# Kernel optimization log

Measured on AMD Instinct MI355X. Metric: run time of the kernel, lower is better.

The kernel has to match this reference:

```python
import jax, jax.numpy as jnp
import numpy as np

EPS = 1e-6

def _rms_norm(t, g):
    # t: [B, S, C] (applied before the view to heads, matching the torch code)
    y = t.astype(jnp.float32)
    y = jax.lax.rsqrt(jnp.mean(y * y, axis=-1, keepdims=True) + EPS)
    return (t * y * g).astype(t.dtype)

def _apply_rope(t, cos, sin):
    # t: [B, S, N, D]; cos/sin: [1, S, 1, D//2]; interleaved pair rotation
    b, s, n, d = t.shape
    tr = t.reshape(b, s, n, d // 2, 2)
    tre, tim = tr[..., 0], tr[..., 1]
    out = jnp.stack([tre * cos - tim * sin, tre * sin + tim * cos], axis=-1)
    return out.reshape(b, s, n, d)

def setup_inputs() -> dict:
    key = jax.random.key(0)
    ks = jax.random.split(key, 8)
    B, S, DIM, N, D = 2, 1024, 3072, 24, 128
    x = jax.random.normal(ks[0], (B, S, DIM), dtype=jnp.float32)
    seq_lens = jax.random.randint(ks[1], (B,), S // 2, S + 1, dtype=jnp.int32)
    grid_sizes = jnp.tile(jnp.array([[16, 8, 8]], dtype=jnp.int32), (B, 1))
    # rope angle table [1024, D//2]: pos * inv_freq
    inv_freq = 1.0 / (10000.0 ** (jnp.arange(D // 2, dtype=jnp.float32) * 2.0 / D))
    freqs = jnp.arange(1024, dtype=jnp.float32)[:, None] * inv_freq[None, :]
    sc = 1.0 / np.sqrt(DIM)
    Wq = jax.random.normal(ks[2], (DIM, DIM), dtype=jnp.float32) * sc
    Wk = jax.random.normal(ks[3], (DIM, DIM), dtype=jnp.float32) * sc
    Wv = jax.random.normal(ks[4], (DIM, DIM), dtype=jnp.float32) * sc
    Wo = jax.random.normal(ks[5], (DIM, DIM), dtype=jnp.float32) * sc
    bq = jnp.zeros((DIM,), jnp.float32); bk = jnp.zeros((DIM,), jnp.float32)
    bv = jnp.zeros((DIM,), jnp.float32); bo = jnp.zeros((DIM,), jnp.float32)
    gq = jnp.ones((DIM,), jnp.float32); gk = jnp.ones((DIM,), jnp.float32)
    return {"x": x, "seq_lens": seq_lens, "grid_sizes": grid_sizes, "freqs": freqs,
            "Wq": Wq, "bq": bq, "Wk": Wk, "bk": bk, "Wv": Wv, "bv": bv,
            "Wo": Wo, "bo": bo, "gq": gq, "gk": gk}

def reference(x, seq_lens, grid_sizes, freqs, Wq, bq, Wk, bk, Wv, bv, Wo, bo, gq, gk):
    b, s, dim = x.shape
    d = 2 * freqs.shape[1]          # head_dim
    n = dim // d                    # num_heads
    q = _rms_norm(x @ Wq.T + bq, gq).reshape(b, s, n, d)
    k = _rms_norm(x @ Wk.T + bk, gk).reshape(b, s, n, d)
    v = (x @ Wv.T + bv).reshape(b, s, n, d)
    ang = freqs[:s]                 # [S, D//2]
    cos = jnp.cos(ang)[None, :, None, :]
    sin = jnp.sin(ang)[None, :, None, :]
    q = _apply_rope(q, cos, sin)
    k = _apply_rope(k, cos, sin)
    # full attention (window_size = (-1,-1)), varlen key masking via seq_lens
    scale = d ** -0.5
    scores = jnp.einsum('bind,bjnd->bnij', q, k) * scale   # [B,N,S,S]
    key_valid = jnp.arange(s)[None, :] < seq_lens[:, None]  # [B,S]
    scores = jnp.where(key_valid[:, None, None, :], scores, jnp.finfo(scores.dtype).min)
    p = jax.nn.softmax(scores, axis=-1)
    out = jnp.einsum('bnij,bjnd->bind', p, v).reshape(b, s, dim)
    return out @ Wo.T + bo
```

## Files before the change

### kernel.cpp

```cpp
#include <hip/hip_runtime.h>
#include <cmath>

#define BB   2
#define SS   1024
#define DIMM 3072
#define NHH  24
#define HDD  128
#define MM   (BB * SS)

typedef _Float16 f16;
typedef __attribute__((ext_vector_type(8))) _Float16 half8;
typedef __attribute__((ext_vector_type(4))) float floatx4;
typedef unsigned int u32;
typedef const __attribute__((address_space(1))) u32* gp1;
typedef __attribute__((address_space(3))) u32* lp3;

__device__ __forceinline__ void gload_lds16(const void* g, void* l) {
    __builtin_amdgcn_global_load_lds((gp1)g, (lp3)l, 16, 0, 0);
}

__global__ __launch_bounds__(256) void cvt_f16_kernel(
    const float* __restrict__ in, f16* __restrict__ outp, int n8)
{
    int i = blockIdx.x * 256 + threadIdx.x;
    if (i >= n8) return;
    const float4* p = (const float4*)(in + (size_t)i * 8);
    float4 a = p[0], b = p[1];
    half8 h = {(f16)a.x, (f16)a.y, (f16)a.z, (f16)a.w,
               (f16)b.x, (f16)b.y, (f16)b.z, (f16)b.w};
    *(half8*)(outp + (size_t)i * 8) = h;
}

template<bool QKV>
__global__ __launch_bounds__(256) void gemm_f16(
    const f16* __restrict__ A,
    const float* __restrict__ W0, const float* __restrict__ W1, const float* __restrict__ W2,
    const float* __restrict__ b0, const float* __restrict__ b1, const float* __restrict__ b2,
    f16* __restrict__ D0, f16* __restrict__ D1, f16* __restrict__ D2,
    float* __restrict__ F)
{
    constexpr int K = DIMM;
    constexpr int NSTEP = K / 32;
    __shared__ f16 As[128 * 32];
    __shared__ f16 Bs[128 * 32];

    const int tid  = threadIdx.x;
    const int lane = tid & 63;
    const int wave = tid >> 6;
    const int wm = wave >> 1, wn = wave & 1;
    const int lr = lane & 15;
    const int lq = lane >> 4;

    const int id  = blockIdx.x;
    const int cpx = (int)gridDim.x >> 3;
    const int swz = (id & 7) * cpx + (id >> 3);
    const int bm = (swz & 15) << 7;
    const int bn = (swz >> 4) << 7;

    const float* W; const float* bias; f16* D = nullptr;
    int nloc = bn;
    if constexpr (QKV) {
        int sel = bn / DIMM;
        nloc = bn - sel * DIMM;
        W    = sel == 0 ? W0 : (sel == 1 ? W1 : W2);
        bias = sel == 0 ? b0 : (sel == 1 ? b1 : b2);
        D    = sel == 0 ? D0 : (sel == 1 ? D1 : D2);
    } else { W = W0; bias = b0; }

    const int r0 = tid >> 2;
    const int c8 = (tid & 3) << 3;
    const float* bp0 = W + (size_t)(nloc + r0) * K + c8;
    const float* bp1 = W + (size_t)(nloc + r0 + 64) * K + c8;

    const int arow_l = lane >> 2;
    const int acol_l = (lane & 3) << 3;
    const f16* agbase = A + (size_t)bm * K;

    float4 sb00, sb01, sb10, sb11;
    auto LOADB = [&](int k0) {
        sb00 = *(const float4*)(bp0 + k0); sb01 = *(const float4*)(bp0 + k0 + 4);
        sb10 = *(const float4*)(bp1 + k0); sb11 = *(const float4*)(bp1 + k0 + 4);
    };
    auto STOREB = [&]() {
        half8 h0 = {(f16)sb00.x, (f16)sb00.y, (f16)sb00.z, (f16)sb00.w,
                    (f16)sb01.x, (f16)sb01.y, (f16)sb01.z, (f16)sb01.w};
        half8 h1 = {(f16)sb10.x, (f16)sb10.y, (f16)sb10.z, (f16)sb10.w,
                    (f16)sb11.x, (f16)sb11.y, (f16)sb11.z, (f16)sb11.w};
        *(half8*)&Bs[r0 * 32 + c8]        = h0;
        *(half8*)&Bs[(r0 + 64) * 32 + c8] = h1;
    };

    floatx4 acc[4][4];
#pragma unroll
    for (int i = 0; i < 4; ++i)
#pragma unroll
        for (int j = 0; j < 4; ++j) acc[i][j] = (floatx4){0.f, 0.f, 0.f, 0.f};

    LOADB(0);
    for (int ks = 0; ks < NSTEP; ++ks) {
        const int k0 = ks * 32;
        __syncthreads();
#pragma unroll
        for (int i = 0; i < 2; ++i) {
            int rbase = wave * 32 + i * 16;
            gload_lds16(agbase + (size_t)(rbase + arow_l) * K + k0 + acol_l,
                        &As[rbase * 32]);
        }
        STOREB();
        __syncthreads();
        if (ks + 1 < NSTEP) LOADB(k0 + 32);

        half8 af[4], bf[4];
#pragma unroll
        for (int i = 0; i < 4; ++i) {
            af[i] = *(const half8*)&As[(wm * 64 + i * 16 + lr) * 32 + lq * 8];
            bf[i] = *(const half8*)&Bs[(wn * 64 + i * 16 + lr) * 32 + lq * 8];
        }
#pragma unroll
        for (int mi = 0; mi < 4; ++mi)
#pragma unroll
            for (int ni = 0; ni < 4; ++ni)
                acc[mi][ni] = __builtin_amdgcn_mfma_f32_16x16x32_f16(af[mi], bf[ni], acc[mi][ni], 0, 0, 0);
    }

    const int crow0 = bm + wm * 64 + (lq << 2);
    const int ccol0 = nloc + wn * 64;
#pragma unroll
    for (int ni = 0; ni < 4; ++ni) {
        const int col = ccol0 + ni * 16 + lr;
        const float bv = bias[col];
#pragma unroll
        for (int mi = 0; mi < 4; ++mi) {
            const int row = crow0 + mi * 16;
#pragma unroll
            for (int r2 = 0; r2 < 4; ++r2) {
                if constexpr (QKV)
                    D[(size_t)(row + r2) * DIMM + col] = (f16)(acc[mi][ni][r2] + bv);
                else
                    F[(size_t)(row + r2) * DIMM + col] = acc[mi][ni][r2] + bv;
            }
        }
    }
}

__global__ __launch_bounds__(192) void rmsnorm_rope_f16(
    f16* __restrict__ q, f16* __restrict__ k,
    const float* __restrict__ gq, const float* __restrict__ gk,
    const float* __restrict__ freqs)
{
    f16* t = (blockIdx.y == 0) ? q : k;
    const float* g = (blockIdx.y == 0) ? gq : gk;
    const int row = blockIdx.x;
    const int s = row & (SS - 1);
    const int tid = threadIdx.x;
    f16* base = t + (size_t)row * DIMM + tid * 16;

    half8 v0 = *(const half8*)base;
    half8 v1 = *(const half8*)(base + 8);
    float v[16];
#pragma unroll
    for (int j = 0; j < 8; ++j) { v[j] = (float)v0[j]; v[8 + j] = (float)v1[j]; }

    float ssq = 0.f;
#pragma unroll
    for (int j = 0; j < 16; ++j) ssq += v[j] * v[j];
#pragma unroll
    for (int off = 32; off > 0; off >>= 1) ssq += __shfl_down(ssq, off, 64);
    __shared__ float red[3];
    if ((tid & 63) == 0) red[tid >> 6] = ssq;
    __syncthreads();
    float tot = red[0] + red[1] + red[2];
    float sc = rsqrtf(tot * (1.0f / (float)DIMM) + 1e-6f);

    const float* gp = g + tid * 16;
    float y[16];
#pragma unroll
    for (int j = 0; j < 16; ++j) y[j] = v[j] * sc * gp[j];

#pragma unroll
    for (int p = 0; p < 8; ++p) {
        int idx = tid * 16 + 2 * p;
        int f = (idx & 127) >> 1;
        float ang = freqs[s * 64 + f];
        float cc = cosf(ang), sn = sinf(ang);
        float e = y[2 * p], o = y[2 * p + 1];
        y[2 * p]     = e * cc - o * sn;
        y[2 * p + 1] = e * sn + o * cc;
    }
    half8 o0, o1;
#pragma unroll
    for (int j = 0; j < 8; ++j) { o0[j] = (f16)y[j]; o1[j] = (f16)y[8 + j]; }
    *(half8*)base       = o0;
    *(half8*)(base + 8) = o1;
}

__global__ __launch_bounds__(256) void flash_attn_f16(
    const f16* __restrict__ Q, const f16* __restrict__ K,
    const f16* __restrict__ V, const int* __restrict__ seq_lens,
    f16* __restrict__ O)
{
    __shared__ f16 QPs[64 * 128];
    __shared__ f16 Ks[64 * 128];
    __shared__ f16 Vt[128 * 64];

    const int tid  = threadIdx.x;
    const int lane = tid & 63;
    const int wave = tid >> 6;
    const int ln = lane & 15;
    const int lq = lane >> 4;
    const int i0 = blockIdx.x * 64;
    const int h  = blockIdx.y;
    const int b  = blockIdx.z;
    const int slen = seq_lens[b];
    const float scale = 0.08838834764831845f;
    const size_t gstride = NHH * HDD;

    const f16* Qg = Q + ((size_t)(b * SS + i0) * NHH + h) * HDD;
#pragma unroll
    for (int rep = 0; rep < 4; ++rep) {
        int u = tid + rep * 256;
        int r = u >> 4, d0 = (u & 15) << 3;
        half8 qv = *(const half8*)(Qg + (size_t)r * gstride + d0);
        *(half8*)(QPs + r * 128 + (d0 ^ ((r & 7) << 3))) = qv;
    }
    __syncthreads();

    half8 qfrag[4];
    {
        int rq = wave * 16 + ln;
#pragma unroll
        for (int ks = 0; ks < 4; ++ks)
            qfrag[ks] = *(const half8*)(QPs + rq * 128 + ((ks * 32 + lq * 8) ^ ((rq & 7) << 3)));
    }

    floatx4 accO[8];
#pragma unroll
    for (int dt = 0; dt < 8; ++dt) accO[dt] = (floatx4){0.f, 0.f, 0.f, 0.f};
    float mrow[4] = {-3.0e38f, -3.0e38f, -3.0e38f, -3.0e38f};
    float lrow[4] = {0.f, 0.f, 0.f, 0.f};

    const int nT = (slen + 63) >> 6;
    for (int t = 0; t < nT; ++t) {
        const int j0g = t * 64;
        __syncthreads();

        const f16* Kg = K + ((size_t)(b * SS + j0g) * NHH + h) * HDD;
#pragma unroll
        for (int rep = 0; rep < 4; ++rep) {
            int u = tid + rep * 256;
            int r = u >> 4, d0 = (u & 15) << 3;
            half8 kv = *(const half8*)(Kg + (size_t)r * gstride + d0);
            *(half8*)(Ks + r * 128 + (d0 ^ ((r & 7) << 3))) = kv;
        }
        const f16* Vg = V + ((size_t)(b * SS + j0g) * NHH + h) * HDD;
#pragma unroll
        for (int rep = 0; rep < 2; ++rep) {
            int u = tid + rep * 256;
            int jp = u & 31, j0 = jp * 2;
            int d0 = (u >> 5) << 3;
            half8 va = *(const half8*)(Vg + (size_t)j0 * gstride + d0);
            half8 vb = *(const half8*)(Vg + (size_t)(j0 + 1) * gstride + d0);
#pragma unroll
            for (int i = 0; i < 8; ++i) {
                int d = d0 + i;
                union { f16 h[2]; u32 w; } pk;
                pk.h[0] = va[i]; pk.h[1] = vb[i];
                *(u32*)(Vt + d * 64 + (j0 ^ ((d & 7) << 3))) = pk.w;
            }
        }
        __syncthreads();

        floatx4 acc_s[4];
#pragma unroll
        for (int nt = 0; nt < 4; ++nt) {
            acc_s[nt] = (floatx4){0.f, 0.f, 0.f, 0.f};
            int rk = nt * 16 + ln;
#pragma unroll
            for (int ks = 0; ks < 4; ++ks) {
                half8 kf = *(const half8*)(Ks + rk * 128 + ((ks * 32 + lq * 8) ^ ((rk & 7) << 3)));
                acc_s[nt] = __builtin_amdgcn_mfma_f32_16x16x32_f16(qfrag[ks], kf, acc_s[nt], 0, 0, 0);
            }
        }

        float s[4][4];
#pragma unroll
        for (int nt = 0; nt < 4; ++nt) {
            int j = j0g + nt * 16 + ln;
            bool valid = (j < slen);
#pragma unroll
            for (int r = 0; r < 4; ++r)
                s[nt][r] = valid ? acc_s[nt][r] * scale : -3.0e38f;
        }
        float fct[4];
#pragma unroll
        for (int r = 0; r < 4; ++r) {
            float m4 = fmaxf(fmaxf(s[0][r], s[1][r]), fmaxf(s[2][r], s[3][r]));
            m4 = fmaxf(m4, __shfl_xor(m4, 1, 64));
            m4 = fmaxf(m4, __shfl_xor(m4, 2, 64));
            m4 = fmaxf(m4, __shfl_xor(m4, 4, 64));
            m4 = fmaxf(m4, __shfl_xor(m4, 8, 64));
            float mn = fmaxf(mrow[r], m4);
            fct[r] = __expf(mrow[r] - mn);
            mrow[r] = mn;
            float ls = 0.f;
#pragma unroll
            for (int nt = 0; nt < 4; ++nt) {
                float p = __expf(s[nt][r] - mn);
                s[nt][r] = p;
                ls += p;
            }
            ls += __shfl_xor(ls, 1, 64);
            ls += __shfl_xor(ls, 2, 64);
            ls += __shfl_xor(ls, 4, 64);
            ls += __shfl_xor(ls, 8, 64);
            lrow[r] = lrow[r] * fct[r] + ls;
        }

#pragma unroll
        for (int nt = 0; nt < 4; ++nt) {
#pragma unroll
            for (int r = 0; r < 4; ++r) {
                int rw = lq * 4 + r;
                int j = nt * 16 + ln;
                QPs[(wave * 16 + rw) * 128 + (j ^ ((rw & 7) << 3))] = (f16)s[nt][r];
            }
        }

#pragma unroll
        for (int dt = 0; dt < 8; ++dt)
#pragma unroll
            for (int r = 0; r < 4; ++r) accO[dt][r] *= fct[r];

        half8 pfrag[2];
#pragma unroll
        for (int js = 0; js < 2; ++js)
            pfrag[js] = *(const half8*)(QPs + (wave * 16 + ln) * 128 + ((js * 32 + lq * 8) ^ ((ln & 7) << 3)));
#pragma unroll
        for (int dt = 0; dt < 8; ++dt) {
            int d = dt * 16 + ln;
#pragma unroll
            for (int js = 0; js < 2; ++js) {
                half8 vf = *(const half8*)(Vt + d * 64 + ((js * 32 + lq * 8) ^ ((d & 7) << 3)));
                accO[dt] = __builtin_amdgcn_mfma_f32_16x16x32_f16(pfrag[js], vf, accO[dt], 0, 0, 0);
            }
        }
    }

    float linv[4];
#pragma unroll
    for (int r = 0; r < 4; ++r) linv[r] = 1.0f / lrow[r];
    f16* Og = O + ((size_t)(b * SS + i0) * NHH + h) * HDD;
#pragma unroll
    for (int dt = 0; dt < 8; ++dt) {
#pragma unroll
        for (int r = 0; r < 4; ++r) {
            int qr = wave * 16 + lq * 4 + r;
            int d = dt * 16 + ln;
            Og[(size_t)qr * gstride + d] = (f16)(accO[dt][r] * linv[r]);
        }
    }
}

extern "C" void kernel_launch(void* const* d_in, const int* in_sizes, int n_in,
                              void* d_out, int out_size, void* d_ws, size_t ws_size,
                              hipStream_t stream)
{
    const float* x     = (const float*)d_in[0];
    const int*   seq   = (const int*)d_in[1];
    const float* freqs = (const float*)d_in[3];
    const float* Wq    = (const float*)d_in[4];
    const float* bq    = (const float*)d_in[5];
    const float* Wk    = (const float*)d_in[6];
    const float* bk    = (const float*)d_in[7];
    const float* Wv    = (const float*)d_in[8];
    const float* bv    = (const float*)d_in[9];
    const float* Wo    = (const float*)d_in[10];
    const float* bo    = (const float*)d_in[11];
    const float* gq    = (const float*)d_in[12];
    const float* gk    = (const float*)d_in[13];

    float* out = (float*)d_out;
    const size_t MD = (size_t)MM * DIMM;

    f16* X16 = (f16*)d_ws;
    f16* q16 = X16 + MD;
    f16* k16 = X16 + 2 * MD;
    f16* v16 = (f16*)d_out;

    cvt_f16_kernel<<<(int)(MD / (256 * 8)), 256, 0, stream>>>(x, X16, (int)(MD / 8));
    gemm_f16<true><<<(MM / 128) * (3 * DIMM / 128), 256, 0, stream>>>(
        X16, Wq, Wk, Wv, bq, bk, bv, q16, k16, v16, nullptr);
    rmsnorm_rope_f16<<<dim3(MM, 2), 192, 0, stream>>>(q16, k16, gq, gk, freqs);
    flash_attn_f16<<<dim3(SS / 64, NHH, BB), 256, 0, stream>>>(q16, k16, v16, seq, X16);
    gemm_f16<false><<<(MM / 128) * (DIMM / 128), 256, 0, stream>>>(
        X16, Wo, nullptr, nullptr, bo, nullptr, nullptr, nullptr, nullptr, nullptr, out);
}
```

Before: 386.7 us.

## Pre-convert weights to f16 and use direct-to-LDS GEMM with swizzled tiles

After: 368.8 us. -4.6%, faster.

```diff
diff --git a/kernel.cpp b/kernel.cpp
--- a/kernel.cpp
+++ b/kernel.cpp
@@ -32,7 +32,103 @@
 }
 
 template<bool QKV>
-__global__ __launch_bounds__(256) void gemm_f16(
+__global__ __launch_bounds__(256) void gemm_f16p(
+    const f16* __restrict__ A,
+    const f16* __restrict__ W0, const f16* __restrict__ W1, const f16* __restrict__ W2,
+    const float* __restrict__ b0, const float* __restrict__ b1, const float* __restrict__ b2,
+    f16* __restrict__ D0, f16* __restrict__ D1, f16* __restrict__ D2,
+    float* __restrict__ F)
+{
+    constexpr int K = DIMM;
+    constexpr int NSTEP = K / 64;
+    __shared__ __align__(16) f16 As[128 * 64];
+    __shared__ __align__(16) f16 Bs[128 * 64];
+
+    const int tid  = threadIdx.x;
+    const int lane = tid & 63;
+    const int wave = tid >> 6;
+    const int wm = wave >> 1, wn = wave & 1;
+    const int lr = lane & 15;
+    const int lq = lane >> 4;
+
+    const int id  = blockIdx.x;
+    const int cpx = (int)gridDim.x >> 3;
+    const int swz = (id & 7) * cpx + (id >> 3);
+    const int bm = (swz & 15) << 7;
+    const int bn = (swz >> 4) << 7;
+
+    const f16* Wh; const float* bias; f16* D = nullptr;
+    int nloc = bn;
+    if constexpr (QKV) {
+        int sel = bn / DIMM;
+        nloc = bn - sel * DIMM;
+        Wh   = sel == 0 ? W0 : (sel == 1 ? W1 : W2);
+        bias = sel == 0 ? b0 : (sel == 1 ? b1 : b2);
+        D    = sel == 0 ? D0 : (sel == 1 ? D1 : D2);
+    } else { Wh = W0; bias = b0; }
+
+    const int srow = lane >> 3;
+    const int scol = ((lane & 7) ^ srow) << 3;
+    const f16* ag = A  + (size_t)(bm   + srow) * K + scol;
+    const f16* bg = Wh + (size_t)(nloc + srow) * K + scol;
+
+    floatx4 acc[4][4];
+#pragma unroll
+    for (int i = 0; i < 4; ++i)
+#pragma unroll
+        for (int j = 0; j < 4; ++j) acc[i][j] = (floatx4){0.f, 0.f, 0.f, 0.f};
+
+    for (int ks = 0; ks < NSTEP; ++ks) {
+        const int k0 = ks * 64;
+        __syncthreads();
+#pragma unroll
+        for (int i = 0; i < 4; ++i) {
+            int rbase = wave * 32 + i * 8;
+            gload_lds16(ag + (size_t)rbase * K + k0, &As[rbase * 64]);
+            gload_lds16(bg + (size_t)rbase * K + k0, &Bs[rbase * 64]);
+        }
+        __syncthreads();
+
+#pragma unroll
+        for (int sub = 0; sub < 2; ++sub) {
+            half8 af[4], bf[4];
+#pragma unroll
+            for (int i = 0; i < 4; ++i) {
+                int ra = wm * 64 + i * 16 + lr;
+                int rb = wn * 64 + i * 16 + lr;
+                af[i] = *(const half8*)&As[ra * 64 + ((((sub << 2) + lq) ^ (lr & 7)) << 3)];
+                bf[i] = *(const half8*)&Bs[rb * 64 + ((((sub << 2) + lq) ^ (lr & 7)) << 3)];
+            }
+#pragma unroll
+            for (int mi = 0; mi < 4; ++mi)
+#pragma unroll
+                for (int ni = 0; ni < 4; ++ni)
+                    acc[mi][ni] = __builtin_amdgcn_mfma_f32_16x16x32_f16(af[mi], bf[ni], acc[mi][ni], 0, 0, 0);
+        }
+    }
+
+    const int crow0 = bm + wm * 64 + (lq << 2);
+    const int ccol0 = nloc + wn * 64;
+#pragma unroll
+    for (int ni = 0; ni < 4; ++ni) {
+        const int col = ccol0 + ni * 16 + lr;
+        const float bv = bias[col];
+#pragma unroll
+        for (int mi = 0; mi < 4; ++mi) {
+            const int row = crow0 + mi * 16;
+#pragma unroll
+            for (int r2 = 0; r2 < 4; ++r2) {
+                if constexpr (QKV)
+                    D[(size_t)(row + r2) * DIMM + col] = (f16)(acc[mi][ni][r2] + bv);
+                else
+                    F[(size_t)(row + r2) * DIMM + col] = acc[mi][ni][r2] + bv;
+            }
+        }
+    }
+}
+
+template<bool QKV>
+__global__ __launch_bounds__(256) void gemm_f16m(
     const f16* __restrict__ A,
     const float* __restrict__ W0, const float* __restrict__ W1, const float* __restrict__ W2,
     const float* __restrict__ b0, const float* __restrict__ b1, const float* __restrict__ b2,
@@ -199,9 +295,9 @@
     const f16* __restrict__ V, const int* __restrict__ seq_lens,
     f16* __restrict__ O)
 {
-    __shared__ f16 QPs[64 * 128];
-    __shared__ f16 Ks[64 * 128];
-    __shared__ f16 Vt[128 * 64];
+    __shared__ __align__(16) f16 QPs[64 * 128];
+    __shared__ __align__(16) f16 Ks[64 * 128];
+    __shared__ __align__(16) f16 Vt[128 * 64];
 
     const int tid  = threadIdx.x;
     const int lane = tid & 63;
@@ -381,17 +477,40 @@
 
     float* out = (float*)d_out;
     const size_t MD = (size_t)MM * DIMM;
+    const size_t WD = (size_t)DIMM * DIMM;
 
     f16* X16 = (f16*)d_ws;
     f16* q16 = X16 + MD;
     f16* k16 = X16 + 2 * MD;
     f16* v16 = (f16*)d_out;
 
-    cvt_f16_kernel<<<(int)(MD / (256 * 8)), 256, 0, stream>>>(x, X16, (int)(MD / 8));
-    gemm_f16<true><<<(MM / 128) * (3 * DIMM / 128), 256, 0, stream>>>(
-        X16, Wq, Wk, Wv, bq, bk, bv, q16, k16, v16, nullptr);
-    rmsnorm_rope_f16<<<dim3(MM, 2), 192, 0, stream>>>(q16, k16, gq, gk, freqs);
-    flash_attn_f16<<<dim3(SS / 64, NHH, BB), 256, 0, stream>>>(q16, k16, v16, seq, X16);
-    gemm_f16<false><<<(MM / 128) * (DIMM / 128), 256, 0, stream>>>(
-        X16, Wo, nullptr, nullptr, bo, nullptr, nullptr, nullptr, nullptr, nullptr, out);
-}
+    const int nMD8 = (int)(MD / 8);
+    const int nWD8 = (int)(WD / 8);
+    const size_t need = (3 * MD + 3 * WD) * sizeof(f16);
+
+    cvt_f16_kernel<<<nMD8 / 256, 256, 0, stream>>>(x, X16, nMD8);
+
+    if (ws_size >= need) {
+        f16* Wq16 = X16 + 3 * MD;
+        f16* Wk16 = Wq16 + WD;
+        f16* Wv16 = Wk16 + WD;
+        f16* Wo16 = Wq16;
+        cvt_f16_kernel<<<nWD8 / 256, 256, 0, stream>>>(Wq, Wq16, nWD8);
+        cvt_f16_kernel<<<nWD8 / 256, 256, 0, stream>>>(Wk, Wk16, nWD8);
+        cvt_f16_kernel<<<nWD8 / 256, 256, 0, stream>>>(Wv, Wv16, nWD8);
+        gemm_f16p<true><<<(MM / 128) * (3 * DIMM / 128), 256, 0, stream>>>(
+            X16, Wq16, Wk16, Wv16, bq, bk, bv, q16, k16, v16, nullptr);
+        cvt_f16_kernel<<<nWD8 / 256, 256, 0, stream>>>(Wo, Wo16, nWD8);
+        rmsnorm_rope_f16<<<dim3(MM, 2), 192, 0, stream>>>(q16, k16, gq, gk, freqs);
+        flash_attn_f16<<<dim3(SS / 64, NHH, BB), 256, 0, stream>>>(q16, k16, v16, seq, X16);
+        gemm_f16p<false><<<(MM / 128) * (DIMM / 128), 256, 0, stream>>>(
+            X16, Wo16, nullptr, nullptr, bo, nullptr, nullptr, nullptr, nullptr, nullptr, out);
+    } else {
+        gemm_f16m<true><<<(MM / 128) * (3 * DIMM / 128), 256, 0, stream>>>(
+            X16, Wq, Wk, Wv, bq, bk, bv, q16, k16, v16, nullptr);
+        rmsnorm_rope_f16<<<dim3(MM, 2), 192, 0, stream>>>(q16, k16, gq, gk, freqs);
+        flash_attn_f16<<<dim3(SS / 64, NHH, BB), 256, 0, stream>>>(q16, k16, v16, seq, X16);
+        gemm_f16m<false><<<(MM / 128) * (DIMM / 128), 256, 0, stream>>>(
+            X16, Wo, nullptr, nullptr, bo, nullptr, nullptr, nullptr, nullptr, nullptr, out);
+    }
+}
```
